# Performance work log

Measured on AMD Instinct MI355X. Metric: run time of the kernel, lower is better.

Reference implementation:

```python
import jax, jax.numpy as jnp
import numpy as np

NUM_HEADS = 8
SPLIT_S = 4
DIM = 288            # n_feat * 3 * 3
SCALE = (DIM // NUM_HEADS) ** -0.5  # quirk: uses full dim's head_dim (36), not reduced
EPS = 1e-5


def _extract_patches(x):
    # x: [B,C,H,W] -> [B, C*9, H*W], 3x3 kernel, stride 1, 'same' padding
    B, C, H, W = x.shape
    xp = jnp.pad(x, ((0, 0), (0, 0), (1, 1), (1, 1)))
    pats = jnp.stack([xp[:, :, i:i + H, j:j + W] for i in range(3) for j in range(3)], axis=2)
    return pats.reshape(B, C * 9, H * W)


def _fold(cols, H, W):
    # inverse of extract: [B, C*9, H*W] -> [B,C,H,W], summing overlapping patches
    B, Ck, _ = cols.shape
    C = Ck // 9
    p = cols.reshape(B, C, 3, 3, H, W)
    out = jnp.zeros((B, C, H + 2, W + 2), cols.dtype)
    for i in range(3):
        for j in range(3):
            out = out.at[:, :, i:i + H, j:j + W].add(p[:, :, i, j])
    return out[:, :, 1:H + 1, 1:W + 1]


def _ln(x, w, b):
    mu = x.mean(-1, keepdims=True)
    var = ((x - mu) ** 2).mean(-1, keepdims=True)
    return (x - mu) * jax.lax.rsqrt(var + EPS) * w + b


def _attn(x, reduce_w, qkv_w, proj_w, proj_b):
    # x: [B,N,288] -> reduce -> [B,N,144] -> block-diag attention over s=4 chunks
    x = x @ reduce_w.T
    B, N, C = x.shape
    hd = C // NUM_HEADS
    qkv = (x @ qkv_w.T).reshape(B, N, 3, NUM_HEADS, hd).transpose(2, 0, 3, 1, 4)
    q, k, v = qkv[0], qkv[1], qkv[2]          # [B,h,N,hd]
    chunk = N // SPLIT_S
    q = q.reshape(B, NUM_HEADS, SPLIT_S, chunk, hd)
    k = k.reshape(B, NUM_HEADS, SPLIT_S, chunk, hd)
    v = v.reshape(B, NUM_HEADS, SPLIT_S, chunk, hd)
    attn = jnp.einsum('bhscd,bhsed->bhsce', q, k) * SCALE   # [B,h,s,chunk,chunk]
    attn = jax.nn.softmax(attn, axis=-1)
    out = jnp.einsum('bhsce,bhsed->bhscd', attn, v)          # [B,h,s,chunk,hd]
    out = out.transpose(0, 2, 3, 1, 4).reshape(B, N, C)      # cat chunks on token dim
    return out @ proj_w.T + proj_b


def setup_inputs() -> dict:
    key = jax.random.key(0)
    ks = jax.random.split(key, 12)
    d, dr, dh = DIM, DIM // 2, DIM // 4  # 288, 144, 72
    f = lambda k, shape: (jax.random.normal(k, shape, jnp.float32) * 0.02)
    return {
        'x': jax.random.normal(ks[0], (4, 32, 64, 64), jnp.float32),
        'ln1_w': jnp.ones((d,), jnp.float32), 'ln1_b': jnp.zeros((d,), jnp.float32),
        'reduce_w': f(ks[1], (dr, d)),
        'qkv_w': f(ks[2], (3 * dr, dr)),
        'proj_w': f(ks[3], (d, dr)), 'proj_b': jnp.zeros((d,), jnp.float32),
        'ln2_w': jnp.ones((d,), jnp.float32), 'ln2_b': jnp.zeros((d,), jnp.float32),
        'fc1_w': f(ks[4], (dh, d)), 'fc1_b': jnp.zeros((dh,), jnp.float32),
        'fc2_w': f(ks[5], (d, dh)), 'fc2_b': jnp.zeros((d,), jnp.float32),
    }


def reference(x, ln1_w, ln1_b, reduce_w, qkv_w, proj_w, proj_b, ln2_w, ln2_b, fc1_w, fc1_b, fc2_w, fc2_b):
    B, C, H, W = x.shape
    t = _extract_patches(x).transpose(0, 2, 1)  # [B, N=H*W, 288]
    t = t + _attn(_ln(t, ln1_w, ln1_b), reduce_w, qkv_w, proj_w, proj_b)
    h = _ln(t, ln2_w, ln2_b)
    t = t + (jax.nn.relu(h @ fc1_w.T + fc1_b) @ fc2_w.T + fc2_b)
    return _fold(t.transpose(0, 2, 1), H, W)
```

## Files before the change

kernel.cpp:

```cpp
#include <hip/hip_runtime.h>
#include <hip/hip_bf16.h>

typedef __hip_bfloat16 bf16;
typedef unsigned short u16;
typedef unsigned int u32;
typedef __attribute__((ext_vector_type(8))) short bf16x8;
typedef __attribute__((ext_vector_type(4))) float f32x4;

#define BB 4
#define CCH 32
#define HH 64
#define WW 64
#define NN 4096
#define D 288
#define DR 144
#define DQ 432
#define NH 8
#define HD 18
#define SPLIT 4
#define CHUNK 1024
#define KS 512
#define DH 72
#define SCALE_ 0.16666666666666666f
#define QSCALE 0.24044917348149343f
#define EPS_ 1e-5f
#define ASTR 160
#define ATS 168
#define HSTR 96

__device__ __attribute__((aligned(16))) u16 g_Wcb[DQ * D];
__device__ __attribute__((aligned(16))) u16 g_pw[D * ASTR];
__device__ __attribute__((aligned(16))) u16 g_f1w[HSTR * D];
__device__ __attribute__((aligned(16))) u16 g_f2w[D * HSTR];
__device__ __attribute__((aligned(16))) u16 g_q[(size_t)BB * NH * NN * 32];
__device__ __attribute__((aligned(16))) u16 g_k[(size_t)BB * NH * NN * 32];
__device__ __attribute__((aligned(16))) u16 g_vt[(size_t)BB * NH * SPLIT * 32 * CHUNK];
__device__ __attribute__((aligned(16))) float g_part[2 * (size_t)BB * NH * NN * 20];
__device__ __attribute__((aligned(16))) u16 g_h[(size_t)BB * NN * HSTR];
__device__ __attribute__((aligned(16))) u16 g_t0[(size_t)BB * NN * D];
__device__ __attribute__((aligned(16))) u16 g_t1[(size_t)BB * NN * D];
__device__ float g_t2[(size_t)BB * D * NN];
__device__ int   g_flag;

__device__ __forceinline__ float b2f(bf16 v) { return __bfloat162float(v); }
__device__ __forceinline__ float bits2f(u16 u) { return __uint_as_float(((u32)u) << 16); }
__device__ __forceinline__ u16 f2bits(float f) {
    u32 u = __float_as_uint(f);
    return (u16)((u + 0x7FFF + ((u >> 16) & 1)) >> 16);
}
__device__ __forceinline__ float ldin(const void* p, size_t i, int isbf) {
    return isbf ? b2f(((const bf16*)p)[i]) : ((const float*)p)[i];
}

#define RS  (D * ASTR + HSTR * D + D * HSTR)
#define RS2 (RS + BB * NH * SPLIT * CHUNK)
#define RSB ((RS2 + 255) / 256)
#define PATCHB (BB * HH)

__global__ void k_prep(const void* __restrict__ x, const void* __restrict__ qkv_w,
                       const void* __restrict__ reduce_w, const void* __restrict__ proj_w,
                       const void* __restrict__ fc1_w, const void* __restrict__ fc2_w) {
    __shared__ int cnt4[4];
    __shared__ float qw[DR];
    __shared__ float slab[32 * 3 * 66];
    int tid = threadIdx.x;
    {
        const u16* u = (const u16*)x;
        int c = 0;
        for (int i = tid; i < 2048; i += 256) c += (((u[i] >> 7) & 0xFF) >= 0x90);
        for (int o = 32; o; o >>= 1) c += __shfl_xor(c, o);
        if ((tid & 63) == 0) cnt4[tid >> 6] = c;
    }
    __syncthreads();
    int bf = (cnt4[0] + cnt4[1] + cnt4[2] + cnt4[3]) < 32;
    if (tid == 0 && blockIdx.x == 0) g_flag = bf;

    int bid = blockIdx.x;
    if (bid < DQ) {
        int o = bid;
        if (tid < DR) qw[tid] = ldin(qkv_w, (size_t)o * DR + tid, bf);
        __syncthreads();
        for (int col = tid; col < D; col += 256) {
            float s0 = 0.f, s1 = 0.f;
            #pragma unroll 4
            for (int j = 0; j < DR; j += 2) {
                s0 += qw[j] * ldin(reduce_w, (size_t)j * D + col, bf);
                s1 += qw[j + 1] * ldin(reduce_w, (size_t)(j + 1) * D + col, bf);
            }
            g_Wcb[(size_t)o * D + col] = f2bits(s0 + s1);
        }
    } else if (bid < DQ + RSB) {
        int idx = (bid - DQ) * 256 + tid;
        if (idx < D * ASTR) {
            int o = idx / ASTR, j = idx % ASTR;
            g_pw[idx] = (j < DR) ? f2bits(ldin(proj_w, (size_t)o * DR + j, bf)) : (u16)0;
        } else if (idx < D * ASTR + HSTR * D) {
            int t = idx - D * ASTR;
            int o = t / D;
            g_f1w[t] = (o < DH) ? f2bits(ldin(fc1_w, (size_t)t, bf)) : (u16)0;
        } else if (idx < RS) {
            int t = idx - D * ASTR - HSTR * D;
            int o = t / HSTR, j = t % HSTR;
            g_f2w[t] = (j < DH) ? f2bits(ldin(fc2_w, (size_t)o * DH + j, bf)) : (u16)0;
        } else if (idx < RS2) {
            int t = idx - RS;
            int bhs = t >> 10, n = t & 1023;
            g_vt[((size_t)bhs * 32 + 18) * CHUNK + n] = 0x3F80;
        }
    } else {
        int pb = bid - DQ - RSB;
        int b = pb >> 6, y = pb & 63;
        for (int idx = tid; idx < 32 * 3 * 66; idx += 256) {
            int c = idx / 198, rem = idx % 198;
            int ki = rem / 66, col = rem % 66 - 1;
            int sy = y + ki - 1;
            float v = 0.f;
            if (col >= 0 && col < 64 && sy >= 0 && sy < 64)
                v = ldin(x, ((size_t)(b * CCH + c) * HH + sy) * WW + col, bf);
            slab[idx] = v;
        }
        __syncthreads();
        size_t obase = ((size_t)b * NN + y * 64) * D;
        for (int idx = tid; idx < 64 * D; idx += 256) {
            int t = idx / D, f = idx % D;
            int c = f / 9, k = f % 9, ki = k / 3, kj = k % 3;
            g_t0[obase + idx] = f2bits(slab[c * 198 + ki * 66 + t + kj]);
        }
    }
}

__global__ void k_ln_qkv(const void* __restrict__ lnw, const void* __restrict__ lnb) {
    __shared__ __attribute__((aligned(16))) u16 xln[16 * 296];
    __shared__ float lnwf[D], lnbf[D];
    __shared__ float smu[16], srs[16];
    __shared__ u16 vbuf[144][18];
    int bf = g_flag;
    int tid = threadIdx.x;
    size_t tok0 = (size_t)blockIdx.x * 16;
    for (int i = tid; i < D; i += 256) { lnwf[i] = ldin(lnw, i, bf); lnbf[i] = ldin(lnb, i, bf); }
    {
        int tt = tid >> 4, p = tid & 15;
        const u32* pr = (const u32*)(g_t0 + (tok0 + tt) * D + p * 18);
        float s = 0.f, q = 0.f;
        #pragma unroll
        for (int j = 0; j < 9; ++j) {
            u32 v = pr[j];
            float a = bits2f((u16)(v & 0xFFFF)), b = bits2f((u16)(v >> 16));
            s += a + b; q += a * a + b * b;
        }
        #pragma unroll
        for (int o = 1; o < 16; o <<= 1) { s += __shfl_xor(s, o); q += __shfl_xor(q, o); }
        if (p == 0) {
            float mu = s / D;
            smu[tt] = mu;
            srs[tt] = rsqrtf(q / D - mu * mu + EPS_);
        }
    }
    __syncthreads();
    for (int idx = tid; idx < 16 * 144; idx += 256) {
        int t = idx / 144, dw = idx % 144;
        u32 v = *(const u32*)(g_t0 + (tok0 + t) * D + 2 * dw);
        float mu = smu[t], rs = srs[t];
        int f = 2 * dw;
        float a = (bits2f((u16)(v & 0xFFFF)) - mu) * rs * lnwf[f] + lnbf[f];
        float b = (bits2f((u16)(v >> 16)) - mu) * rs * lnwf[f + 1] + lnbf[f + 1];
        *(u32*)&xln[t * 296 + f] = (u32)f2bits(a) | ((u32)f2bits(b) << 16);
    }
    __syncthreads();
    int w = tid >> 6, lane = tid & 63, quad = lane >> 4, l15 = lane & 15;
    bf16x8 areg[9];
    const u16* abase = xln + l15 * 296 + quad * 8;
    #pragma unroll
    for (int ks = 0; ks < 9; ++ks) areg[ks] = *(const bf16x8*)(abase + ks * 32);
    int nt0 = w * 7, nt1 = (nt0 + 7 > 27) ? 27 : nt0 + 7;
    for (int nt = nt0; nt < nt1; ++nt) {
        f32x4 acc = {0.f, 0.f, 0.f, 0.f};
        const u16* bbase = g_Wcb + (size_t)(nt * 16 + l15) * D + quad * 8;
        #pragma unroll
        for (int ks = 0; ks < 9; ++ks) {
            bf16x8 bfr = *(const bf16x8*)(bbase + ks * 32);
            acc = __builtin_amdgcn_mfma_f32_16x16x32_bf16(areg[ks], bfr, acc, 0, 0, 0);
        }
        int o = nt * 16 + l15;
        int which = o / DR, rem = o % DR, hh = rem / HD, dd = rem % HD;
        #pragma unroll
        for (int r = 0; r < 4; ++r) {
            size_t token = tok0 + quad * 4 + r;
            int b_ = (int)(token >> 12), n = (int)(token & 4095);
            size_t row = (size_t)(b_ * NH + hh) * NN + n;
            if (which == 0)      g_q[row * 32 + dd] = f2bits(acc[r] * QSCALE);
            else if (which == 1) g_k[row * 32 + dd] = f2bits(acc[r]);
            else                 vbuf[rem][quad * 4 + r] = f2bits(acc[r]);
        }
    }
    __syncthreads();
    {
        int b_ = (int)(tok0 >> 12);
        int n0 = (int)(tok0 & 4095);
        int sIdx = n0 >> 10, nc = n0 & 1023;
        for (int idx = tid; idx < 144 * 16; idx += 256) {
            int rem = idx >> 4, t = idx & 15;
            int hh = rem / HD, dd = rem % HD;
            size_t voff = (((size_t)(b_ * NH + hh) * SPLIT + sIdx) * 32 + dd) * CHUNK + nc + t;
            g_vt[voff] = vbuf[rem][t];
        }
    }
}

#define PSTR 72
__global__ __launch_bounds__(128) void k_attn() {
    __shared__ __attribute__((aligned(16))) u16 Pl[2][4][16 * PSTR];
    int bid = blockIdx.x;
    int chunk = bid & 127;
    int qblk = (bid >> 7) & 7;
    int ksl = bid >> 10;
    int s = chunk & 3, bh = chunk >> 2;
    int tid = threadIdx.x;
    int w = tid >> 6, lane = tid & 63, quad = lane >> 4, l15 = lane & 15;

    size_t rowbase = (size_t)bh * NN + s * CHUNK;
    size_t vtbase = ((size_t)bh * SPLIT + s) * 32 * CHUNK;
    const u16* kbase = g_k + rowbase * 32 + quad * 8;
    const u16* vbase = g_vt + vtbase + quad * 8;

    int qbase = qblk * 128 + w * 64;
    bf16x8 qf[4];
    #pragma unroll
    for (int t = 0; t < 4; ++t)
        qf[t] = *(const bf16x8*)(g_q + (rowbase + qbase + t * 16 + l15) * 32 + quad * 8);

    f32x4 accA[4], accB[4];
    #pragma unroll
    for (int t = 0; t < 4; ++t) {
        accA[t] = (f32x4){0.f, 0.f, 0.f, 0.f};
        accB[t] = (f32x4){0.f, 0.f, 0.f, 0.f};
    }

    int kt0 = ksl * KS;
    for (int kk = 0; kk < KS; kk += 64) {
        int kt = kt0 + kk;
        bf16x8 kf0 = *(const bf16x8*)(kbase + (size_t)(kt + 2 * l15) * 32);
        bf16x8 kf1 = *(const bf16x8*)(kbase + (size_t)(kt + 2 * l15 + 1) * 32);
        bf16x8 kf2 = *(const bf16x8*)(kbase + (size_t)(kt + 32 + 2 * l15) * 32);
        bf16x8 kf3 = *(const bf16x8*)(kbase + (size_t)(kt + 33 + 2 * l15) * 32);
        bf16x8 vA0 = *(const bf16x8*)(vbase + (size_t)l15 * CHUNK + kt);
        bf16x8 vB0 = *(const bf16x8*)(vbase + (size_t)(16 + l15) * CHUNK + kt);
        bf16x8 vA1 = *(const bf16x8*)(vbase + (size_t)l15 * CHUNK + kt + 32);
        bf16x8 vB1 = *(const bf16x8*)(vbase + (size_t)(16 + l15) * CHUNK + kt + 32);
        f32x4 z = {0.f, 0.f, 0.f, 0.f};
        #pragma unroll
        for (int t = 0; t < 4; ++t) {
            u16* pw = Pl[w][t];
            f32x4 S0 = __builtin_amdgcn_mfma_f32_16x16x32_bf16(qf[t], kf0, z, 0, 0, 0);
            f32x4 S1 = __builtin_amdgcn_mfma_f32_16x16x32_bf16(qf[t], kf1, z, 0, 0, 0);
            f32x4 S2 = __builtin_amdgcn_mfma_f32_16x16x32_bf16(qf[t], kf2, z, 0, 0, 0);
            f32x4 S3 = __builtin_amdgcn_mfma_f32_16x16x32_bf16(qf[t], kf3, z, 0, 0, 0);
            #pragma unroll
            for (int r = 0; r < 4; ++r) {
                float p0 = exp2f(S0[r]), p1 = exp2f(S1[r]);
                float p2 = exp2f(S2[r]), p3 = exp2f(S3[r]);
                u32 w0 = __builtin_amdgcn_perm(__float_as_uint(p1), __float_as_uint(p0), 0x07060302u);
                u32 w1 = __builtin_amdgcn_perm(__float_as_uint(p3), __float_as_uint(p2), 0x07060302u);
                *(u32*)&pw[(quad * 4 + r) * PSTR + 2 * l15] = w0;
                *(u32*)&pw[(quad * 4 + r) * PSTR + 32 + 2 * l15] = w1;
            }
        }
        #pragma unroll
        for (int t = 0; t < 4; ++t) {
            const u16* pw = Pl[w][t];
            bf16x8 pf0 = *(const bf16x8*)&pw[l15 * PSTR + quad * 8];
            bf16x8 pf1 = *(const bf16x8*)&pw[l15 * PSTR + 32 + quad * 8];
            accA[t] = __builtin_amdgcn_mfma_f32_16x16x32_bf16(pf0, vA0, accA[t], 0, 0, 0);
            accB[t] = __builtin_amdgcn_mfma_f32_16x16x32_bf16(pf0, vB0, accB[t], 0, 0, 0);
            accA[t] = __builtin_amdgcn_mfma_f32_16x16x32_bf16(pf1, vA1, accA[t], 0, 0, 0);
            accB[t] = __builtin_amdgcn_mfma_f32_16x16x32_bf16(pf1, vB1, accB[t], 0, 0, 0);
        }
    }
    float* pb = g_part + (((size_t)ksl * 32 + bh) * SPLIT + s) * (size_t)(CHUNK * 20);
    #pragma unroll
    for (int t = 0; t < 4; ++t) {
        #pragma unroll
        for (int r = 0; r < 4; ++r) {
            int tokenc = qbase + t * 16 + quad * 4 + r;
            float* row = pb + (size_t)tokenc * 20;
            row[l15] = accA[t][r];
            if (l15 < 3) row[16 + l15] = accB[t][r];
        }
    }
}

__global__ void k_proj_ln_fc1(const void* __restrict__ proj_b, const void* __restrict__ lnw,
                              const void* __restrict__ lnb, const void* __restrict__ fc1_b) {
    __shared__ float t1f[16][290];
    __shared__ __attribute__((aligned(16))) u16 xln[16 * 296];
    __shared__ __attribute__((aligned(16))) u16 attnT[16 * ATS];
    __shared__ float linv[16][8];
    __shared__ float lnwf[D], lnbf[D];
    __shared__ float smu[16], srs[16];
    int bf = g_flag;
    int tid = threadIdx.x;
    size_t tok0 = (size_t)blockIdx.x * 16;
    int w = tid >> 6, lane = tid & 63, quad = lane >> 4, l15 = lane & 15;
    for (int i = tid; i < D; i += 256) { lnwf[i] = ldin(lnw, i, bf); lnbf[i] = ldin(lnb, i, bf); }

    int b_ = (int)(tok0 >> 12);
    int s_ = ((int)tok0 & 4095) >> 10;
    int tc0 = (int)tok0 & 1023;
    if (tid < 128) {
        int t = tid >> 3, h = tid & 7;
        const float* p1 = g_part + (((size_t)(b_ * NH + h)) * SPLIT + s_) * (size_t)(CHUNK * 20)
                        + (size_t)(tc0 + t) * 20;
        const float* p2 = p1 + (size_t)32 * SPLIT * CHUNK * 20;
        linv[t][h] = 1.f / (p1[18] + p2[18]);
    }
    __syncthreads();
    for (int idx = tid; idx < 16 * ATS; idx += 256) {
        int t = idx / ATS, f = idx - t * ATS;
        u16 v = 0;
        if (f < DR) {
            int h = f / HD, d = f - h * HD;
            const float* p1 = g_part + (((size_t)(b_ * NH + h)) * SPLIT + s_) * (size_t)(CHUNK * 20)
                            + (size_t)(tc0 + t) * 20;
            const float* p2 = p1 + (size_t)32 * SPLIT * CHUNK * 20;
            v = f2bits((p1[d] + p2[d]) * linv[t][h]);
        }
        attnT[idx] = v;
    }
    __syncthreads();

    {
        bf16x8 areg[5];
        const u16* abase = attnT + l15 * ATS + quad * 8;
        #pragma unroll
        for (int ks = 0; ks < 5; ++ks) areg[ks] = *(const bf16x8*)(abase + ks * 32);
        const int tab[5] = {0, 5, 10, 14, 18};
        for (int nt = tab[w]; nt < tab[w + 1]; ++nt) {
            f32x4 acc = {0.f, 0.f, 0.f, 0.f};
            const u16* bbase = g_pw + (size_t)(nt * 16 + l15) * ASTR + quad * 8;
            #pragma unroll
            for (int ks = 0; ks < 5; ++ks) {
                bf16x8 bfr = *(const bf16x8*)(bbase + ks * 32);
                acc = __builtin_amdgcn_mfma_f32_16x16x32_bf16(areg[ks], bfr, acc, 0, 0, 0);
            }
            int o = nt * 16 + l15;
            float bias = ldin(proj_b, o, bf);
            #pragma unroll
            for (int r = 0; r < 4; ++r) {
                size_t token = tok0 + quad * 4 + r;
                size_t off = token * D + o;
                float val = bits2f(g_t0[off]) + acc[r] + bias;
                g_t1[off] = f2bits(val);
                t1f[quad * 4 + r][o] = val;
            }
        }
    }
    __syncthreads();
    {
        int tt = tid >> 4, p = tid & 15;
        const float* src = &t1f[tt][p * 18];
        float s = 0.f, q = 0.f;
        #pragma unroll
        for (int j = 0; j < 18; ++j) { float a = src[j]; s += a; q += a * a; }
        #pragma unroll
        for (int o = 1; o < 16; o <<= 1) { s += __shfl_xor(s, o); q += __shfl_xor(q, o); }
        if (p == 0) {
            float mu = s / D;
            smu[tt] = mu;
            srs[tt] = rsqrtf(q / D - mu * mu + EPS_);
        }
    }
    __syncthreads();
    for (int idx = tid; idx < 16 * 144; idx += 256) {
        int t = idx / 144, dw = idx % 144;
        int f = 2 * dw;
        float mu = smu[t], rs = srs[t];
        float a = (t1f[t][f] - mu) * rs * lnwf[f] + lnbf[f];
        float b = (t1f[t][f + 1] - mu) * rs * lnwf[f + 1] + lnbf[f + 1];
        *(u32*)&xln[t * 296 + f] = (u32)f2bits(a) | ((u32)f2bits(b) << 16);
    }
    __syncthreads();
    {
        bf16x8 areg[9];
        const u16* abase = xln + l15 * 296 + quad * 8;
        #pragma unroll
        for (int ks = 0; ks < 9; ++ks) areg[ks] = *(const bf16x8*)(abase + ks * 32);
        const int tab2[5] = {0, 2, 4, 5, 6};
        for (int nt = tab2[w]; nt < tab2[w + 1]; ++nt) {
            f32x4 acc = {0.f, 0.f, 0.f, 0.f};
            const u16* bbase = g_f1w + (size_t)(nt * 16 + l15) * D + quad * 8;
            #pragma unroll
            for (int ks = 0; ks < 9; ++ks) {
                bf16x8 bfr = *(const bf16x8*)(bbase + ks * 32);
                acc = __builtin_amdgcn_mfma_f32_16x16x32_bf16(areg[ks], bfr, acc, 0, 0, 0);
            }
            int o = nt * 16 + l15;
            float bias = (o < DH) ? ldin(fc1_b, o, bf) : 0.f;
            #pragma unroll
            for (int r = 0; r < 4; ++r) {
                size_t token = tok0 + quad * 4 + r;
                g_h[token * HSTR + o] = f2bits(fmaxf(acc[r] + bias, 0.f));
            }
        }
    }
}

__global__ void k_fc2(const void* __restrict__ fc2_b) {
    __shared__ float t2f[16][293];
    int bf = g_flag;
    int tid = threadIdx.x;
    size_t tok0 = (size_t)blockIdx.x * 16;
    int w = tid >> 6, lane = tid & 63, quad = lane >> 4, l15 = lane & 15;
    bf16x8 areg[3];
    const u16* abase = g_h + (tok0 + l15) * HSTR + quad * 8;
    #pragma unroll
    for (int ks = 0; ks < 3; ++ks) areg[ks] = *(const bf16x8*)(abase + ks * 32);
    const int tab[5] = {0, 5, 10, 14, 18};
    for (int nt = tab[w]; nt < tab[w + 1]; ++nt) {
        f32x4 acc = {0.f, 0.f, 0.f, 0.f};
        const u16* bbase = g_f2w + (size_t)(nt * 16 + l15) * HSTR + quad * 8;
        #pragma unroll
        for (int ks = 0; ks < 3; ++ks) {
            bf16x8 bfr = *(const bf16x8*)(bbase + ks * 32);
            acc = __builtin_amdgcn_mfma_f32_16x16x32_bf16(areg[ks], bfr, acc, 0, 0, 0);
        }
        int o = nt * 16 + l15;
        float bias = ldin(fc2_b, o, bf);
        #pragma unroll
        for (int r = 0; r < 4; ++r) {
            size_t token = tok0 + quad * 4 + r;
            t2f[quad * 4 + r][o] = bits2f(g_t1[token * D + o]) + acc[r] + bias;
        }
    }
    __syncthreads();
    int b_ = (int)(tok0 >> 12), n0 = (int)(tok0 & 4095);
    for (int idx = tid; idx < D * 16; idx += 256) {
        int o = idx >> 4, t = idx & 15;
        g_t2[((size_t)b_ * D + o) * NN + n0 + t] = t2f[t][o];
    }
}

__global__ void k_fold(void* __restrict__ out) {
    int bf = g_flag;
    int idx = blockIdx.x * blockDim.x + threadIdx.x;
    if (idx >= BB * CCH * HH * WW) return;
    int xx = idx % WW;
    int y = (idx / WW) % HH;
    int c = (idx / (WW * HH)) % CCH;
    int b = idx / (WW * HH * CCH);
    const float* base = g_t2 + ((size_t)b * D + c * 9) * NN;
    float s = 0.f;
    #pragma unroll
    for (int i = 0; i < 3; ++i) {
        int sy = y + 1 - i;
        if (sy < 0 || sy >= HH) continue;
        #pragma unroll
        for (int j = 0; j < 3; ++j) {
            int sx = xx + 1 - j;
            if (sx < 0 || sx >= WW) continue;
            s += base[(size_t)(i * 3 + j) * NN + sy * WW + sx];
        }
    }
    if (bf) ((bf16*)out)[idx] = __float2bfloat16(s);
    else    ((float*)out)[idx] = s;
}

extern "C" void kernel_launch(void* const* d_in, const int* in_sizes, int n_in,
                              void* d_out, int out_size, void* d_ws, size_t ws_size,
                              hipStream_t stream) {
    const void* x        = d_in[0];
    const void* ln1_w    = d_in[1];
    const void* ln1_b    = d_in[2];
    const void* reduce_w = d_in[3];
    const void* qkv_w    = d_in[4];
    const void* proj_w   = d_in[5];
    const void* proj_b   = d_in[6];
    const void* ln2_w    = d_in[7];
    const void* ln2_b    = d_in[8];
    const void* fc1_w    = d_in[9];
    const void* fc1_b    = d_in[10];
    const void* fc2_w    = d_in[11];
    const void* fc2_b    = d_in[12];

    k_prep        <<<DQ + RSB + PATCHB, 256, 0, stream>>>(x, qkv_w, reduce_w, proj_w, fc1_w, fc2_w);
    k_ln_qkv      <<<BB * NN / 16, 256, 0, stream>>>(ln1_w, ln1_b);
    k_attn        <<<2 * BB * NH * SPLIT * 8, 128, 0, stream>>>();
    k_proj_ln_fc1 <<<BB * NN / 16, 256, 0, stream>>>(proj_b, ln2_w, ln2_b, fc1_b);
    k_fc2         <<<BB * NN / 16, 256, 0, stream>>>(fc2_b);
    k_fold        <<<(BB * CCH * HH * WW + 255) / 256, 256, 0, stream>>>(d_out);
}
```

Before: 220.3 us.

## Stage QKV outputs in shared memory, vectorize global stores, store t2 as bf16

The QKV kernel now buffers all of q, k and v in shared memory and writes them to global memory as packed 32-bit stores, replacing scattered 16-bit stores. The attention-combine step in the proj kernel reads the partial results with 128-bit vector loads per (token, head) and drops one barrier and the linv staging. The intermediate t2 before fold is stored as bf16 instead of fp32, which halves that write and read traffic. The bf16 intermediate adds rounding error before the fold summation.

```diff
diff --git a/kernel.cpp b/kernel.cpp
--- a/kernel.cpp
+++ b/kernel.cpp
@@ -39,7 +39,7 @@
 __device__ __attribute__((aligned(16))) u16 g_h[(size_t)BB * NN * HSTR];
 __device__ __attribute__((aligned(16))) u16 g_t0[(size_t)BB * NN * D];
 __device__ __attribute__((aligned(16))) u16 g_t1[(size_t)BB * NN * D];
-__device__ float g_t2[(size_t)BB * D * NN];
+__device__ __attribute__((aligned(16))) u16 g_t2b[(size_t)BB * D * NN];
 __device__ int   g_flag;
 
 __device__ __forceinline__ float b2f(bf16 v) { return __bfloat162float(v); }
@@ -133,7 +133,7 @@
     __shared__ __attribute__((aligned(16))) u16 xln[16 * 296];
     __shared__ float lnwf[D], lnbf[D];
     __shared__ float smu[16], srs[16];
-    __shared__ u16 vbuf[144][18];
+    __shared__ u16 buf[3][144][16];
     int bf = g_flag;
     int tid = threadIdx.x;
     size_t tok0 = (size_t)blockIdx.x * 16;
@@ -182,27 +182,32 @@
             acc = __builtin_amdgcn_mfma_f32_16x16x32_bf16(areg[ks], bfr, acc, 0, 0, 0);
         }
         int o = nt * 16 + l15;
-        int which = o / DR, rem = o % DR, hh = rem / HD, dd = rem % HD;
-        #pragma unroll
-        for (int r = 0; r < 4; ++r) {
-            size_t token = tok0 + quad * 4 + r;
-            int b_ = (int)(token >> 12), n = (int)(token & 4095);
-            size_t row = (size_t)(b_ * NH + hh) * NN + n;
-            if (which == 0)      g_q[row * 32 + dd] = f2bits(acc[r] * QSCALE);
-            else if (which == 1) g_k[row * 32 + dd] = f2bits(acc[r]);
-            else                 vbuf[rem][quad * 4 + r] = f2bits(acc[r]);
-        }
+        int which = o / DR, rem = o % DR;
+        #pragma unroll
+        for (int r = 0; r < 4; ++r)
+            buf[which][rem][quad * 4 + r] = f2bits(which == 0 ? acc[r] * QSCALE : acc[r]);
     }
     __syncthreads();
     {
         int b_ = (int)(tok0 >> 12);
         int n0 = (int)(tok0 & 4095);
         int sIdx = n0 >> 10, nc = n0 & 1023;
-        for (int idx = tid; idx < 144 * 16; idx += 256) {
-            int rem = idx >> 4, t = idx & 15;
+        for (int idx = tid; idx < 2 * 8 * 16 * 9; idx += 256) {
+            int which = idx / 1152;
+            int r2 = idx - which * 1152;
+            int h = r2 / 144, r3 = r2 % 144, t = r3 / 9, dw = r3 % 9;
+            u32 lo = buf[which][h * 18 + 2 * dw][t];
+            u32 hi = buf[which][h * 18 + 2 * dw + 1][t];
+            u16* dst = (which ? g_k : g_q) + ((size_t)(b_ * NH + h) * NN + n0 + t) * 32 + 2 * dw;
+            *(u32*)dst = lo | (hi << 16);
+        }
+        for (int idx = tid; idx < 144 * 8; idx += 256) {
+            int rem = idx >> 3, tp = idx & 7;
             int hh = rem / HD, dd = rem % HD;
-            size_t voff = (((size_t)(b_ * NH + hh) * SPLIT + sIdx) * 32 + dd) * CHUNK + nc + t;
-            g_vt[voff] = vbuf[rem][t];
+            u32 lo = buf[2][rem][2 * tp];
+            u32 hi = buf[2][rem][2 * tp + 1];
+            size_t voff = (((size_t)(b_ * NH + hh) * SPLIT + sIdx) * 32 + dd) * CHUNK + nc + 2 * tp;
+            *(u32*)&g_vt[voff] = lo | (hi << 16);
         }
     }
 }
@@ -294,7 +299,6 @@
     __shared__ float t1f[16][290];
     __shared__ __attribute__((aligned(16))) u16 xln[16 * 296];
     __shared__ __attribute__((aligned(16))) u16 attnT[16 * ATS];
-    __shared__ float linv[16][8];
     __shared__ float lnwf[D], lnbf[D];
     __shared__ float smu[16], srs[16];
     int bf = g_flag;
@@ -306,25 +310,31 @@
     int b_ = (int)(tok0 >> 12);
     int s_ = ((int)tok0 & 4095) >> 10;
     int tc0 = (int)tok0 & 1023;
+    for (int idx = tid; idx < 16 * (ATS - DR); idx += 256) {
+        int t = idx / (ATS - DR), f = idx % (ATS - DR);
+        attnT[t * ATS + DR + f] = 0;
+    }
     if (tid < 128) {
         int t = tid >> 3, h = tid & 7;
         const float* p1 = g_part + (((size_t)(b_ * NH + h)) * SPLIT + s_) * (size_t)(CHUNK * 20)
                         + (size_t)(tc0 + t) * 20;
         const float* p2 = p1 + (size_t)32 * SPLIT * CHUNK * 20;
-        linv[t][h] = 1.f / (p1[18] + p2[18]);
-    }
-    __syncthreads();
-    for (int idx = tid; idx < 16 * ATS; idx += 256) {
-        int t = idx / ATS, f = idx - t * ATS;
-        u16 v = 0;
-        if (f < DR) {
-            int h = f / HD, d = f - h * HD;
-            const float* p1 = g_part + (((size_t)(b_ * NH + h)) * SPLIT + s_) * (size_t)(CHUNK * 20)
-                            + (size_t)(tc0 + t) * 20;
-            const float* p2 = p1 + (size_t)32 * SPLIT * CHUNK * 20;
-            v = f2bits((p1[d] + p2[d]) * linv[t][h]);
-        }
-        attnT[idx] = v;
+        f32x4 a0 = *(const f32x4*)p1,        c0 = *(const f32x4*)p2;
+        f32x4 a1 = *(const f32x4*)(p1 + 4),  c1 = *(const f32x4*)(p2 + 4);
+        f32x4 a2 = *(const f32x4*)(p1 + 8),  c2 = *(const f32x4*)(p2 + 8);
+        f32x4 a3 = *(const f32x4*)(p1 + 12), c3 = *(const f32x4*)(p2 + 12);
+        f32x4 a4 = *(const f32x4*)(p1 + 16), c4 = *(const f32x4*)(p2 + 16);
+        float inv = 1.f / (a4[2] + c4[2]);
+        u16* dst = attnT + t * ATS + h * HD;
+        #pragma unroll
+        for (int d = 0; d < 4; ++d) {
+            dst[d]      = f2bits((a0[d] + c0[d]) * inv);
+            dst[4 + d]  = f2bits((a1[d] + c1[d]) * inv);
+            dst[8 + d]  = f2bits((a2[d] + c2[d]) * inv);
+            dst[12 + d] = f2bits((a3[d] + c3[d]) * inv);
+        }
+        dst[16] = f2bits((a4[0] + c4[0]) * inv);
+        dst[17] = f2bits((a4[1] + c4[1]) * inv);
     }
     __syncthreads();
 
@@ -433,9 +443,10 @@
     }
     __syncthreads();
     int b_ = (int)(tok0 >> 12), n0 = (int)(tok0 & 4095);
-    for (int idx = tid; idx < D * 16; idx += 256) {
-        int o = idx >> 4, t = idx & 15;
-        g_t2[((size_t)b_ * D + o) * NN + n0 + t] = t2f[t][o];
+    for (int idx = tid; idx < D * 8; idx += 256) {
+        int o = idx >> 3, tp = idx & 7;
+        u32 v = (u32)f2bits(t2f[2 * tp][o]) | ((u32)f2bits(t2f[2 * tp + 1][o]) << 16);
+        *(u32*)&g_t2b[((size_t)b_ * D + o) * NN + n0 + 2 * tp] = v;
     }
 }
 
@@ -447,7 +458,7 @@
     int y = (idx / WW) % HH;
     int c = (idx / (WW * HH)) % CCH;
     int b = idx / (WW * HH * CCH);
-    const float* base = g_t2 + ((size_t)b * D + c * 9) * NN;
+    const u16* base = g_t2b + ((size_t)b * D + c * 9) * NN;
     float s = 0.f;
     #pragma unroll
     for (int i = 0; i < 3; ++i) {
@@ -457,7 +468,7 @@
         for (int j = 0; j < 3; ++j) {
             int sx = xx + 1 - j;
             if (sx < 0 || sx >= WW) continue;
-            s += base[(size_t)(i * 3 + j) * NN + sy * WW + sx];
+            s += bits2f(base[(size_t)(i * 3 + j) * NN + sy * WW + sx]);
         }
     }
     if (bf) ((bf16*)out)[idx] = __float2bfloat16(s);
```

Measured after the change: 218.2 us. Within noise of the previous version (-1.0%).
